# Kernel tuning notes

Hardware: AMD Instinct MI355X
Metric: run time of the kernel (lower is better)

## Reference

```python
import jax, jax.numpy as jnp
import numpy as np
from jax import lax

B, L, H = 2, 2048, 768
I = 2 * H            # intermediate_size = 1536
N = 16               # ssm state size
DT_RANK = 48         # ceil(H / 16)
K = 4                # conv kernel


def setup_inputs() -> dict:
    key = jax.random.key(0)
    ks = jax.random.split(key, 10)
    s = lambda fan_in: 1.0 / np.sqrt(fan_in)
    inp = {
        "input_states": jax.random.normal(ks[0], (B, L, H), jnp.float32),
        "in_proj_w": jax.random.normal(ks[1], (H, 2 * I), jnp.float32) * s(H),
        "conv_w": jax.random.normal(ks[2], (I, 1, K), jnp.float32) * s(K),
        "conv_b": jax.random.normal(ks[3], (I,), jnp.float32) * 0.02,
        "x_proj_w": jax.random.normal(ks[4], (I, DT_RANK + 2 * N), jnp.float32) * s(I),
        "dt_proj_w": jax.random.normal(ks[5], (DT_RANK, I), jnp.float32) * s(DT_RANK),
        "dt_proj_b": jax.random.normal(ks[6], (I,), jnp.float32) * 0.1,
        "A_log": jnp.log(jnp.broadcast_to(jnp.arange(1, N + 1, dtype=jnp.float32), (I, N))),
        "D_param": jnp.ones((I,), jnp.float32),
        "out_proj_w": jax.random.normal(ks[7], (I, H), jnp.float32) * s(I),
    }
    return inp


def reference(input_states, in_proj_w, conv_w, conv_b, x_proj_w,
              dt_proj_w, dt_proj_b, A_log, D_param, out_proj_w):
    dtype = input_states.dtype
    # in_proj -> [B, 2I, L], split into hidden and gate
    proj = jnp.einsum("blh,hj->bjl", input_states, in_proj_w)
    hidden, gate = jnp.split(proj, 2, axis=1)              # each [B, I, L]
    # causal depthwise conv1d (padding K-1 then truncate to L == left pad)
    k = conv_w.shape[-1]
    conv_out = lax.conv_general_dilated(
        hidden, conv_w, window_strides=(1,), padding=[(k - 1, 0)],
        feature_group_count=hidden.shape[1],
        dimension_numbers=("NCH", "OIH", "NCH"))
    hidden = jax.nn.silu(conv_out + conv_b[None, :, None])  # [B, I, L]
    # x_proj: [B, L, dt_rank + 2N]
    ssm_p = jnp.einsum("bil,ij->blj", hidden, x_proj_w)
    time_step = ssm_p[..., :DT_RANK]
    Bm = ssm_p[..., DT_RANK:DT_RANK + N]                    # [B, L, N]
    Cm = ssm_p[..., DT_RANK + N:]                           # [B, L, N]
    dt = jax.nn.softplus(time_step @ dt_proj_w + dt_proj_b)  # [B, L, I]
    dt = jnp.transpose(dt, (0, 2, 1))                        # [B, I, L]
    A = -jnp.exp(A_log.astype(jnp.float32))                  # [I, N]
    discrete_A = jnp.exp(A[None, :, None, :] * dt[:, :, :, None])        # [B,I,L,N]
    deltaB_u = (dt[:, :, :, None] * Bm[:, None, :, :].astype(jnp.float32)
                * hidden[:, :, :, None].astype(jnp.float32))             # [B,I,L,N]

    def step(state, x):
        dA_t, dBu_t = x
        new_state = dA_t * state + dBu_t
        return new_state, new_state

    init = jnp.zeros((hidden.shape[0], hidden.shape[1], N), jnp.float32)
    _, states = lax.scan(step, init,
                         (jnp.moveaxis(discrete_A, 2, 0),
                          jnp.moveaxis(deltaB_u, 2, 0)))    # [L, B, I, N]
    y = jnp.einsum("lbin,bln->bil", states, Cm.astype(jnp.float32)).astype(dtype)
    y = y + hidden * D_param[None, :, None]
    y = y * jax.nn.silu(gate)
    return jnp.einsum("bil,ih->blh", y, out_proj_w)
```

## Files before the change

kernel.cpp:

```cpp
#include <hip/hip_runtime.h>
#include <hip/hip_bf16.h>
#include <math.h>

#define B_ 2
#define L_ 2048
#define H_ 768
#define I_ 1536
#define J2 3072
#define KSPLIT 12
#define KCH (I_ / KSPLIT)
#define LC 16
#define NC (L_ / LC)

typedef __bf16 bf16x8 __attribute__((ext_vector_type(8)));
typedef float  f32x4  __attribute__((ext_vector_type(4)));

__device__ __forceinline__ float sigmoidf_(float x) { return 1.f / (1.f + __expf(-x)); }

__global__ __launch_bounds__(256) void pk_cvt(const float* __restrict__ src,
                                              __bf16* __restrict__ dst, int n8)
{
    int idx = blockIdx.x * 256 + threadIdx.x;
    if (idx >= n8) return;
    const float4* s = (const float4*)(src + (size_t)idx * 8);
    float4 a = s[0], b = s[1];
    bf16x8 v = {(__bf16)a.x,(__bf16)a.y,(__bf16)a.z,(__bf16)a.w,
                (__bf16)b.x,(__bf16)b.y,(__bf16)b.z,(__bf16)b.w};
    *(bf16x8*)(dst + (size_t)idx * 8) = v;
}

__global__ __launch_bounds__(256) void pk_tr(const float* __restrict__ src,
    __bf16* __restrict__ dst, int R, int C)
{
    __shared__ float tile[64][65];
    const int c0 = blockIdx.x * 64, r0 = blockIdx.y * 64;
    const int t = threadIdx.x;
    const int cc = t & 63, r4 = t >> 6;
#pragma unroll
    for (int q = 0; q < 16; ++q) {
        int r = r0 + q * 4 + r4;
        if (r < R && c0 + cc < C)
            tile[q * 4 + r4][cc] = src[(size_t)r * C + c0 + cc];
    }
    __syncthreads();
#pragma unroll
    for (int q = 0; q < 16; ++q) {
        int c = c0 + q * 4 + r4;
        if (c < C && r0 + cc < R)
            dst[(size_t)c * R + r0 + cc] = (__bf16)tile[cc][q * 4 + r4];
    }
}

__global__ __launch_bounds__(256) void pk_dtw(const float* __restrict__ dtW,
    __bf16* __restrict__ dtWT)
{
    int idx = blockIdx.x * 256 + threadIdx.x;
    if (idx >= I_ * 64) return;
    int i = idx >> 6, r = idx & 63;
    dtWT[idx] = (r < 48) ? (__bf16)dtW[(size_t)r * I_ + i] : (__bf16)0.f;
}

__global__ __launch_bounds__(256) void k1_mfma(const __bf16* __restrict__ Abf,
    const __bf16* __restrict__ WT, __bf16* __restrict__ preH16, __bf16* __restrict__ g16)
{
    __shared__ __align__(16) char smem[20480];
    __bf16* As = (__bf16*)smem;
    __bf16* Bs = As + 128 * 40;
    const int t = threadIdx.x;
    const int lane = t & 63, w = t >> 6;
    const int wr = w >> 1, wc = w & 1;
    const int m0 = blockIdx.y * 128, n0 = blockIdx.x * 128;
    const int l16 = lane & 15, kb = (lane >> 4) * 8;
    const int arow = t >> 1, ahalf = (t & 1) * 16;
    f32x4 acc[4][4] = {};

    for (int k0 = 0; k0 < H_; k0 += 32) {
        {
            const bf16x8* ap = (const bf16x8*)(Abf + (size_t)(m0 + arow) * H_ + k0 + ahalf);
            *(bf16x8*)&As[arow * 40 + ahalf] = ap[0];
            *(bf16x8*)&As[arow * 40 + ahalf + 8] = ap[1];
            const bf16x8* bp = (const bf16x8*)(WT + (size_t)(n0 + arow) * H_ + k0 + ahalf);
            *(bf16x8*)&Bs[arow * 40 + ahalf] = bp[0];
            *(bf16x8*)&Bs[arow * 40 + ahalf + 8] = bp[1];
        }
        __syncthreads();
        bf16x8 aF[4], bF[4];
#pragma unroll
        for (int mi = 0; mi < 4; ++mi)
            aF[mi] = *(const bf16x8*)&As[(wr * 64 + mi * 16 + l16) * 40 + kb];
#pragma unroll
        for (int ni = 0; ni < 4; ++ni)
            bF[ni] = *(const bf16x8*)&Bs[(wc * 64 + ni * 16 + l16) * 40 + kb];
#pragma unroll
        for (int mi = 0; mi < 4; ++mi)
#pragma unroll
            for (int ni = 0; ni < 4; ++ni)
                acc[mi][ni] = __builtin_amdgcn_mfma_f32_16x16x32_bf16(aF[mi], bF[ni], acc[mi][ni], 0, 0, 0);
        __syncthreads();
    }

    float* slab = (float*)smem + w * 1088;
    const int jtile = n0 + wc * 64;
    const int rm = lane >> 2, jb = (lane & 3) * 16;
    __bf16* outb = (jtile < I_) ? preH16 : g16;
    const int jg = (jtile < I_) ? jtile + jb : jtile - I_ + jb;
#pragma unroll
    for (int mi = 0; mi < 4; ++mi) {
#pragma unroll
        for (int ni = 0; ni < 4; ++ni)
#pragma unroll
            for (int r = 0; r < 4; ++r)
                slab[((lane >> 4) * 4 + r) * 68 + ni * 16 + l16] = acc[mi][ni][r];
        float v[16];
#pragma unroll
        for (int q = 0; q < 16; ++q) v[q] = slab[rm * 68 + jb + q];
        const size_t m = (size_t)m0 + wr * 64 + mi * 16 + rm;
        bf16x8 p0 = {(__bf16)v[0],(__bf16)v[1],(__bf16)v[2],(__bf16)v[3],
                     (__bf16)v[4],(__bf16)v[5],(__bf16)v[6],(__bf16)v[7]};
        bf16x8 p1 = {(__bf16)v[8],(__bf16)v[9],(__bf16)v[10],(__bf16)v[11],
                     (__bf16)v[12],(__bf16)v[13],(__bf16)v[14],(__bf16)v[15]};
        *(bf16x8*)(outb + m * I_ + jg) = p0;
        *(bf16x8*)(outb + m * I_ + jg + 8) = p1;
    }
}

__global__ __launch_bounds__(256) void k2conv(const __bf16* __restrict__ pre,
    const float* __restrict__ cw, const float* __restrict__ cb, __bf16* __restrict__ actT)
{
    __shared__ __bf16 in[67][72];
    const int i0 = blockIdx.x * 64, m0 = blockIdx.y * 64;
    const int l0 = m0 & (L_ - 1);
    const int t = threadIdx.x;
    const int ic = t & 63, r4 = t >> 6;
#pragma unroll
    for (int q = 0; q < 17; ++q) {
        int idx = t + 256 * q;
        if (idx < 67 * 64) {
            int row = idx >> 6, col = idx & 63;
            int lr = l0 - 3 + row;
            __bf16 v = (__bf16)0.f;
            if (lr >= 0)
                v = pre[(size_t)(m0 - 3 + row) * I_ + i0 + col];
            in[row][col] = v;
        }
    }
    __syncthreads();
    const int i = i0 + ic;
    float w0 = cw[i * 4 + 0], w1 = cw[i * 4 + 1], w2 = cw[i * 4 + 2], w3 = cw[i * 4 + 3];
    float bias = cb[i];
#pragma unroll
    for (int q = 0; q < 16; ++q) {
        int mr = q * 4 + r4;
        float s = bias + w0 * (float)in[mr][ic] + w1 * (float)in[mr + 1][ic]
                       + w2 * (float)in[mr + 2][ic] + w3 * (float)in[mr + 3][ic];
        actT[(size_t)(m0 + mr) * I_ + i] = (__bf16)(s * sigmoidf_(s));
    }
}

__global__ __launch_bounds__(256) void k3_split(const __bf16* __restrict__ At,
    const __bf16* __restrict__ XWT, float* __restrict__ part)
{
    __shared__ __align__(16) __bf16 As[64 * 40];
    __shared__ __align__(16) __bf16 Bs[80 * 40];
    const int t = threadIdx.x;
    const int lane = t & 63, w = t >> 6;
    const int m0 = blockIdx.x * 64;
    const int ks = blockIdx.y;
    const int l16 = lane & 15, kb = (lane >> 4) * 8;
    const int arow = t >> 2, aq = (t & 3) * 8;
    f32x4 acc[5] = {};

    for (int k0 = ks * KCH; k0 < (ks + 1) * KCH; k0 += 32) {
        *(bf16x8*)&As[arow * 40 + aq] =
            *(const bf16x8*)(At + (size_t)(m0 + arow) * I_ + k0 + aq);
        if (t < 160) {
            int j = t >> 1, ah = (t & 1) * 16;
            const bf16x8* bp = (const bf16x8*)(XWT + (size_t)j * I_ + k0 + ah);
            *(bf16x8*)&Bs[j * 40 + ah] = bp[0];
            *(bf16x8*)&Bs[j * 40 + ah + 8] = bp[1];
        }
        __syncthreads();
        bf16x8 aF = *(const bf16x8*)&As[(w * 16 + l16) * 40 + kb];
#pragma unroll
        for (int ni = 0; ni < 5; ++ni) {
            bf16x8 bF = *(const bf16x8*)&Bs[(ni * 16 + l16) * 40 + kb];
            acc[ni] = __builtin_amdgcn_mfma_f32_16x16x32_bf16(aF, bF, acc[ni], 0, 0, 0);
        }
        __syncthreads();
    }
    const int mrow = m0 + w * 16 + (lane >> 4) * 4;
    float* pp = part + (size_t)ks * ((size_t)B_ * L_ * 80);
#pragma unroll
    for (int ni = 0; ni < 5; ++ni)
#pragma unroll
        for (int r = 0; r < 4; ++r)
            pp[(size_t)(mrow + r) * 80 + ni * 16 + l16] = acc[ni][r];
}

__global__ __launch_bounds__(256) void k3_reduce(const float* __restrict__ part,
    __bf16* __restrict__ ssm16, float* __restrict__ Bpf, float* __restrict__ Cpf)
{
    int idx = blockIdx.x * 256 + threadIdx.x;
    if (idx >= B_ * L_ * 80) return;
    int m = idx / 80, j = idx - m * 80;
    float s = 0.f;
#pragma unroll
    for (int ks = 0; ks < KSPLIT; ++ks)
        s += part[(size_t)ks * ((size_t)B_ * L_ * 80) + idx];
    if (j < 48) {
        ssm16[(size_t)m * 64 + j] = (__bf16)s;
    } else {
        int n = j & 15;
        if (j < 64) {
            Bpf[(size_t)m * 16 + n] = s;
        } else {
            Cpf[(size_t)m * 16 + n] = s;
            ssm16[(size_t)m * 64 + (j - 16)] = (__bf16)0.f;
        }
    }
}

__global__ __launch_bounds__(256) void k4_mfma(const __bf16* __restrict__ S16,
    const __bf16* __restrict__ dtWT, const float* __restrict__ dtb, __bf16* __restrict__ dt)
{
    __shared__ __align__(16) __bf16 As[128 * 72];
    __shared__ __align__(16) __bf16 Bs[128 * 72];
    const int t = threadIdx.x;
    const int lane = t & 63, w = t >> 6;
    const int wr = w >> 1, wc = w & 1;
    const int m0 = blockIdx.y * 128, n0 = blockIdx.x * 128;
    const int l16 = lane & 15, kq8 = (lane >> 4) * 8;
    {
        const int row = t >> 1, off = (t & 1) * 32;
        const bf16x8* ap = (const bf16x8*)(S16 + (size_t)(m0 + row) * 64 + off);
        *(bf16x8*)&As[row * 72 + off]      = ap[0];
        *(bf16x8*)&As[row * 72 + off + 8]  = ap[1];
        *(bf16x8*)&As[row * 72 + off + 16] = ap[2];
        *(bf16x8*)&As[row * 72 + off + 24] = ap[3];
        const bf16x8* bp = (const bf16x8*)(dtWT + (size_t)(n0 + row) * 64 + off);
        *(bf16x8*)&Bs[row * 72 + off]      = bp[0];
        *(bf16x8*)&Bs[row * 72 + off + 8]  = bp[1];
        *(bf16x8*)&Bs[row * 72 + off + 16] = bp[2];
        *(bf16x8*)&Bs[row * 72 + off + 24] = bp[3];
    }
    __syncthreads();
    f32x4 acc[4][4] = {};
#pragma unroll
    for (int ks = 0; ks < 2; ++ks) {
        const int kb = ks * 32 + kq8;
        bf16x8 aF[4], bF[4];
#pragma unroll
        for (int mi = 0; mi < 4; ++mi)
            aF[mi] = *(const bf16x8*)&As[(wr * 64 + mi * 16 + l16) * 72 + kb];
#pragma unroll
        for (int ni = 0; ni < 4; ++ni)
            bF[ni] = *(const bf16x8*)&Bs[(wc * 64 + ni * 16 + l16) * 72 + kb];
#pragma unroll
        for (int mi = 0; mi < 4; ++mi)
#pragma unroll
            for (int ni = 0; ni < 4; ++ni)
                acc[mi][ni] = __builtin_amdgcn_mfma_f32_16x16x32_bf16(aF[mi], bF[ni], acc[mi][ni], 0, 0, 0);
    }
    const int mbase = m0 + wr * 64 + (lane >> 4) * 4;
    const int nbase = n0 + wc * 64 + l16;
#pragma unroll
    for (int ni = 0; ni < 4; ++ni) {
        const int i = nbase + ni * 16;
        const float bias = dtb[i];
#pragma unroll
        for (int mi = 0; mi < 4; ++mi)
#pragma unroll
            for (int r = 0; r < 4; ++r) {
                float x = acc[mi][ni][r] + bias;
                float sp = (x > 20.f) ? x : log1pf(__expf(x));
                dt[(size_t)(mbase + mi * 16 + r) * I_ + i] = (__bf16)sp;
            }
    }
}

__global__ __launch_bounds__(256) void k5a(const __bf16* __restrict__ dt,
    const __bf16* __restrict__ hT, const float* __restrict__ Bpf,
    float* __restrict__ Ebuf, float* __restrict__ Pbuf)
{
    const int mc = blockIdx.x;
    const int b = mc >> 7, c = mc & (NC - 1);
    const int it = blockIdx.y * 256 + threadIdx.x;
    const int ch = b * I_ + it;
    const size_t mrow0 = (size_t)b * L_ + (size_t)c * LC;

    float s[16];
#pragma unroll
    for (int n = 0; n < 16; ++n) s[n] = 0.f;
    float sumd = 0.f;

    for (int ll = 0; ll < LC; ++ll) {
        const size_t m = mrow0 + ll;
        float d = (float)dt[m * I_ + it];
        float h = (float)hT[m * I_ + it];
        f32x4 B0 = *(const f32x4*)(Bpf + m * 16);
        f32x4 B1 = *(const f32x4*)(Bpf + m * 16 + 4);
        f32x4 B2 = *(const f32x4*)(Bpf + m * 16 + 8);
        f32x4 B3 = *(const f32x4*)(Bpf + m * 16 + 12);
        float u = d * h;
        float e1 = __expf(-d);
        float e2 = e1 * e1, e4 = e2 * e2, e8 = e4 * e4;
        float dA[16];
        dA[0] = e1; dA[1] = e2; dA[2] = e2 * e1; dA[3] = e4;
#pragma unroll
        for (int n = 0; n < 4; ++n) dA[4 + n] = dA[n] * e4;
#pragma unroll
        for (int n = 0; n < 8; ++n) dA[8 + n] = dA[n] * e8;
        sumd += d;
#pragma unroll
        for (int n = 0; n < 16; ++n) {
            float Bn = (n < 4) ? B0[n] : (n < 8) ? B1[n - 4] : (n < 12) ? B2[n - 8] : B3[n - 12];
            s[n] = fmaf(dA[n], s[n], u * Bn);
        }
    }
#pragma unroll
    for (int n = 0; n < 16; ++n)
        Ebuf[(size_t)(c * 16 + n) * J2 + ch] = s[n];
    Pbuf[(size_t)c * J2 + ch] = __expf(-sumd);
}

__global__ __launch_bounds__(256) void k5b(float* __restrict__ Ebuf,
    const float* __restrict__ Pbuf)
{
    const int n = blockIdx.x / (J2 / 256);
    const int ch = (blockIdx.x % (J2 / 256)) * 256 + threadIdx.x;
    const int e = n + 1;
    float run = 0.f;
    for (int c = 0; c < NC; ++c) {
        float E = Ebuf[(size_t)(c * 16 + n) * J2 + ch];
        float f1 = Pbuf[(size_t)c * J2 + ch];
        float pw = 1.f, base = f1;
        int ee = e;
#pragma unroll
        for (int k = 0; k < 5; ++k) {
            if (ee & 1) pw *= base;
            base *= base;
            ee >>= 1;
        }
        Ebuf[(size_t)(c * 16 + n) * J2 + ch] = run;
        run = fmaf(pw, run, E);
    }
}

__global__ __launch_bounds__(256) void k5c(const __bf16* __restrict__ dt,
    __bf16* hyT, const __bf16* __restrict__ g16,
    const float* __restrict__ Bpf, const float* __restrict__ Cpf,
    const float* __restrict__ Ebuf, const float* __restrict__ Dp)
{
    const int mc = blockIdx.x;
    const int b = mc >> 7, c = mc & (NC - 1);
    const int it = blockIdx.y * 256 + threadIdx.x;
    const int ch = b * I_ + it;
    const size_t mrow0 = (size_t)b * L_ + (size_t)c * LC;
    const float D = Dp[it];

    float s[16];
#pragma unroll
    for (int n = 0; n < 16; ++n)
        s[n] = Ebuf[(size_t)(c * 16 + n) * J2 + ch];

    for (int ll = 0; ll < LC; ++ll) {
        const size_t m = mrow0 + ll;
        float d = (float)dt[m * I_ + it];
        float h = (float)hyT[m * I_ + it];
        f32x4 B0 = *(const f32x4*)(Bpf + m * 16);
        f32x4 B1 = *(const f32x4*)(Bpf + m * 16 + 4);
        f32x4 B2 = *(const f32x4*)(Bpf + m * 16 + 8);
        f32x4 B3 = *(const f32x4*)(Bpf + m * 16 + 12);
        f32x4 C0 = *(const f32x4*)(Cpf + m * 16);
        f32x4 C1 = *(const f32x4*)(Cpf + m * 16 + 4);
        f32x4 C2 = *(const f32x4*)(Cpf + m * 16 + 8);
        f32x4 C3 = *(const f32x4*)(Cpf + m * 16 + 12);
        float u = d * h;
        float e1 = __expf(-d);
        float e2 = e1 * e1, e4 = e2 * e2, e8 = e4 * e4;
        float dA[16];
        dA[0] = e1; dA[1] = e2; dA[2] = e2 * e1; dA[3] = e4;
#pragma unroll
        for (int n = 0; n < 4; ++n) dA[4 + n] = dA[n] * e4;
#pragma unroll
        for (int n = 0; n < 8; ++n) dA[8 + n] = dA[n] * e8;
        float a0 = D * h, a1 = 0.f, a2 = 0.f, a3 = 0.f;
#pragma unroll
        for (int n = 0; n < 4; ++n) {
            s[n]      = fmaf(dA[n],      s[n],      u * B0[n]);
            s[n + 4]  = fmaf(dA[n + 4],  s[n + 4],  u * B1[n]);
            s[n + 8]  = fmaf(dA[n + 8],  s[n + 8],  u * B2[n]);
            s[n + 12] = fmaf(dA[n + 12], s[n + 12], u * B3[n]);
            a0 = fmaf(s[n],      C0[n], a0);
            a1 = fmaf(s[n + 4],  C1[n], a1);
            a2 = fmaf(s[n + 8],  C2[n], a2);
            a3 = fmaf(s[n + 12], C3[n], a3);
        }
        float y = (a0 + a1) + (a2 + a3);
        float g = (float)g16[m * I_ + it];
        hyT[m * I_ + it] = (__bf16)(y * g * sigmoidf_(g));
    }
}

__global__ __launch_bounds__(256) void k6_mfma(const __bf16* __restrict__ Yt,
    const __bf16* __restrict__ WoT, float* __restrict__ out)
{
    __shared__ __align__(16) __bf16 As[64 * 40];
    __shared__ __align__(16) __bf16 Bs[64 * 40];
    const int t = threadIdx.x;
    const int lane = t & 63, w = t >> 6;
    const int wr = w >> 1, wc = w & 1;
    const int m0 = blockIdx.y * 64, n0 = blockIdx.x * 64;
    const int l16 = lane & 15, kb = (lane >> 4) * 8;
    const int arow = t >> 2, aq = (t & 3) * 8;
    f32x4 acc[2][2] = {};

    for (int k0 = 0; k0 < I_; k0 += 32) {
        *(bf16x8*)&As[arow * 40 + aq] =
            *(const bf16x8*)(Yt + (size_t)(m0 + arow) * I_ + k0 + aq);
        *(bf16x8*)&Bs[arow * 40 + aq] =
            *(const bf16x8*)(WoT + (size_t)(n0 + arow) * I_ + k0 + aq);
        __syncthreads();
        bf16x8 aF[2], bF[2];
#pragma unroll
        for (int mi = 0; mi < 2; ++mi)
            aF[mi] = *(const bf16x8*)&As[(wr * 32 + mi * 16 + l16) * 40 + kb];
#pragma unroll
        for (int ni = 0; ni < 2; ++ni)
            bF[ni] = *(const bf16x8*)&Bs[(wc * 32 + ni * 16 + l16) * 40 + kb];
#pragma unroll
        for (int mi = 0; mi < 2; ++mi)
#pragma unroll
            for (int ni = 0; ni < 2; ++ni)
                acc[mi][ni] = __builtin_amdgcn_mfma_f32_16x16x32_bf16(aF[mi], bF[ni], acc[mi][ni], 0, 0, 0);
        __syncthreads();
    }
    const int mbase = m0 + wr * 32 + (lane >> 4) * 4;
    const int nbase = n0 + wc * 32 + l16;
#pragma unroll
    for (int mi = 0; mi < 2; ++mi)
#pragma unroll
        for (int ni = 0; ni < 2; ++ni)
#pragma unroll
            for (int r = 0; r < 4; ++r)
                out[(size_t)(mbase + mi * 16 + r) * H_ + nbase + ni * 16] = acc[mi][ni][r];
}

extern "C" void kernel_launch(void* const* d_in, const int* in_sizes, int n_in,
                              void* d_out, int out_size, void* d_ws, size_t ws_size,
                              hipStream_t stream)
{
    const float* in_states  = (const float*)d_in[0];
    const float* in_proj_w  = (const float*)d_in[1];
    const float* conv_w     = (const float*)d_in[2];
    const float* conv_b     = (const float*)d_in[3];
    const float* x_proj_w   = (const float*)d_in[4];
    const float* dt_proj_w  = (const float*)d_in[5];
    const float* dt_proj_b  = (const float*)d_in[6];
    const float* D_param    = (const float*)d_in[8];
    const float* out_proj_w = (const float*)d_in[9];
    float* out = (float*)d_out;

    const size_t CH = (size_t)B_ * I_ * L_;
    const size_t ML = (size_t)B_ * L_;

    char* ws = (char*)d_ws;
    __bf16* dt16  = (__bf16*)ws;
    __bf16* Abf   = (__bf16*)ws;
    __bf16* W1T   = Abf + (size_t)ML * H_;
    char* p = ws + CH * 4;
    __bf16* preH16 = (__bf16*)p;  p += CH * 2;
    __bf16* g16    = (__bf16*)p;  p += CH * 2;
    __bf16* actT   = (__bf16*)p;  p += CH * 2;
    __bf16* ssm16  = (__bf16*)p;  p += ML * 64 * 2;
    float*  Ebuf   = (float*)p;
    float*  part   = (float*)p;
    float*  Pbuf   = Ebuf + (size_t)NC * 16 * J2; p += ((size_t)NC * 16 * J2 + (size_t)NC * J2) * 4;
    __bf16* WoT    = (__bf16*)p;  p += (size_t)H_ * I_ * 2;
    __bf16* XWT    = (__bf16*)p;  p += (size_t)80 * I_ * 2;
    __bf16* dtWT   = (__bf16*)p;  p += (size_t)I_ * 64 * 2;
    float*  Bpf    = (float*)p;   p += ML * 16 * 4;
    float*  Cpf    = (float*)p;

    hipLaunchKernelGGL(pk_cvt, dim3((int)((ML * H_ / 8 + 255) / 256)), dim3(256), 0, stream,
                       in_states, Abf, (int)(ML * H_ / 8));
    hipLaunchKernelGGL(pk_tr, dim3(J2 / 64, H_ / 64), dim3(256), 0, stream,
                       in_proj_w, W1T, H_, J2);
    hipLaunchKernelGGL(pk_tr, dim3(H_ / 64, I_ / 64), dim3(256), 0, stream,
                       out_proj_w, WoT, I_, H_);
    hipLaunchKernelGGL(pk_tr, dim3(2, I_ / 64), dim3(256), 0, stream,
                       x_proj_w, XWT, I_, 80);
    hipLaunchKernelGGL(pk_dtw, dim3((I_ * 64 + 255) / 256), dim3(256), 0, stream,
                       dt_proj_w, dtWT);

    hipLaunchKernelGGL(k1_mfma, dim3(J2 / 128, ML / 128), dim3(256), 0, stream,
                       Abf, W1T, preH16, g16);
    hipLaunchKernelGGL(k2conv, dim3(I_ / 64, ML / 64), dim3(256), 0, stream,
                       preH16, conv_w, conv_b, actT);
    hipLaunchKernelGGL(k3_split, dim3(ML / 64, KSPLIT), dim3(256), 0, stream,
                       actT, XWT, part);
    hipLaunchKernelGGL(k3_reduce, dim3((int)((ML * 80 + 255) / 256)), dim3(256), 0, stream,
                       part, ssm16, Bpf, Cpf);
    hipLaunchKernelGGL(k4_mfma, dim3(I_ / 128, ML / 128), dim3(256), 0, stream,
                       ssm16, dtWT, dt_proj_b, dt16);
    hipLaunchKernelGGL(k5a, dim3(B_ * NC, I_ / 256), dim3(256), 0, stream,
                       dt16, actT, Bpf, Ebuf, Pbuf);
    hipLaunchKernelGGL(k5b, dim3(16 * (J2 / 256)), dim3(256), 0, stream,
                       Ebuf, Pbuf);
    hipLaunchKernelGGL(k5c, dim3(B_ * NC, I_ / 256), dim3(256), 0, stream,
                       dt16, actT, g16, Bpf, Cpf, Ebuf, D_param);
    hipLaunchKernelGGL(k6_mfma, dim3(H_ / 64, ML / 64), dim3(256), 0, stream,
                       actT, WoT, out);
}
```

Measured before the change: 218.9 us.

## Merge weight prep kernels, swizzle GEMM tiles, and double scan chunk length

```diff
diff --git a/kernel.cpp b/kernel.cpp
--- a/kernel.cpp
+++ b/kernel.cpp
@@ -9,7 +9,7 @@
 #define J2 3072
 #define KSPLIT 12
 #define KCH (I_ / KSPLIT)
-#define LC 16
+#define LC 32
 #define NC (L_ / LC)
 
 typedef __bf16 bf16x8 __attribute__((ext_vector_type(8)));
@@ -17,24 +17,10 @@
 
 __device__ __forceinline__ float sigmoidf_(float x) { return 1.f / (1.f + __expf(-x)); }
 
-__global__ __launch_bounds__(256) void pk_cvt(const float* __restrict__ src,
-                                              __bf16* __restrict__ dst, int n8)
-{
-    int idx = blockIdx.x * 256 + threadIdx.x;
-    if (idx >= n8) return;
-    const float4* s = (const float4*)(src + (size_t)idx * 8);
-    float4 a = s[0], b = s[1];
-    bf16x8 v = {(__bf16)a.x,(__bf16)a.y,(__bf16)a.z,(__bf16)a.w,
-                (__bf16)b.x,(__bf16)b.y,(__bf16)b.z,(__bf16)b.w};
-    *(bf16x8*)(dst + (size_t)idx * 8) = v;
-}
-
-__global__ __launch_bounds__(256) void pk_tr(const float* __restrict__ src,
-    __bf16* __restrict__ dst, int R, int C)
-{
-    __shared__ float tile[64][65];
-    const int c0 = blockIdx.x * 64, r0 = blockIdx.y * 64;
-    const int t = threadIdx.x;
+__device__ __forceinline__ void tr_tile_(const float* __restrict__ src,
+    __bf16* __restrict__ dst, int R, int C, int bx, int by, int t, float (*tile)[65])
+{
+    const int c0 = bx * 64, r0 = by * 64;
     const int cc = t & 63, r4 = t >> 6;
 #pragma unroll
     for (int q = 0; q < 16; ++q) {
@@ -51,13 +37,36 @@
     }
 }
 
-__global__ __launch_bounds__(256) void pk_dtw(const float* __restrict__ dtW,
-    __bf16* __restrict__ dtWT)
-{
-    int idx = blockIdx.x * 256 + threadIdx.x;
-    if (idx >= I_ * 64) return;
-    int i = idx >> 6, r = idx & 63;
-    dtWT[idx] = (r < 48) ? (__bf16)dtW[(size_t)r * I_ + i] : (__bf16)0.f;
+__global__ __launch_bounds__(256) void pk_all(
+    const float* __restrict__ in_states, __bf16* __restrict__ Abf,
+    const float* __restrict__ in_proj_w, __bf16* __restrict__ W1T,
+    const float* __restrict__ out_proj_w, __bf16* __restrict__ WoT,
+    const float* __restrict__ x_proj_w, __bf16* __restrict__ XWT,
+    const float* __restrict__ dt_proj_w, __bf16* __restrict__ dtWT)
+{
+    __shared__ float tile[64][65];
+    const int bb = blockIdx.x, t = threadIdx.x;
+    if (bb < 1536) {
+        int idx = bb * 256 + t;
+        const float4* s = (const float4*)(in_states + (size_t)idx * 8);
+        float4 a = s[0], b = s[1];
+        bf16x8 v = {(__bf16)a.x,(__bf16)a.y,(__bf16)a.z,(__bf16)a.w,
+                    (__bf16)b.x,(__bf16)b.y,(__bf16)b.z,(__bf16)b.w};
+        *(bf16x8*)(Abf + (size_t)idx * 8) = v;
+    } else if (bb < 2112) {
+        int idx = bb - 1536;
+        tr_tile_(in_proj_w, W1T, H_, J2, idx % 48, idx / 48, t, tile);
+    } else if (bb < 2400) {
+        int idx = bb - 2112;
+        tr_tile_(out_proj_w, WoT, I_, H_, idx % 12, idx / 12, t, tile);
+    } else if (bb < 2448) {
+        int idx = bb - 2400;
+        tr_tile_(x_proj_w, XWT, I_, 80, idx % 2, idx / 2, t, tile);
+    } else {
+        int idx = (bb - 2448) * 256 + t;
+        int i = idx >> 6, r = idx & 63;
+        dtWT[idx] = (r < 48) ? (__bf16)dt_proj_w[(size_t)r * I_ + i] : (__bf16)0.f;
+    }
 }
 
 __global__ __launch_bounds__(256) void k1_mfma(const __bf16* __restrict__ Abf,
@@ -69,7 +78,9 @@
     const int t = threadIdx.x;
     const int lane = t & 63, w = t >> 6;
     const int wr = w >> 1, wc = w & 1;
-    const int m0 = blockIdx.y * 128, n0 = blockIdx.x * 128;
+    const int flat = blockIdx.y * 24 + blockIdx.x;
+    const int swz = (flat & 7) * 96 + (flat >> 3);
+    const int m0 = (swz / 24) * 128, n0 = (swz % 24) * 128;
     const int l16 = lane & 15, kb = (lane >> 4) * 8;
     const int arow = t >> 1, ahalf = (t & 1) * 16;
     f32x4 acc[4][4] = {};
@@ -283,7 +294,7 @@
     float* __restrict__ Ebuf, float* __restrict__ Pbuf)
 {
     const int mc = blockIdx.x;
-    const int b = mc >> 7, c = mc & (NC - 1);
+    const int b = mc / NC, c = mc & (NC - 1);
     const int it = blockIdx.y * 256 + threadIdx.x;
     const int ch = b * I_ + it;
     const size_t mrow0 = (size_t)b * L_ + (size_t)c * LC;
@@ -352,7 +363,7 @@
     const float* __restrict__ Ebuf, const float* __restrict__ Dp)
 {
     const int mc = blockIdx.x;
-    const int b = mc >> 7, c = mc & (NC - 1);
+    const int b = mc / NC, c = mc & (NC - 1);
     const int it = blockIdx.y * 256 + threadIdx.x;
     const int ch = b * I_ + it;
     const size_t mrow0 = (size_t)b * L_ + (size_t)c * LC;
@@ -410,7 +421,9 @@
     const int t = threadIdx.x;
     const int lane = t & 63, w = t >> 6;
     const int wr = w >> 1, wc = w & 1;
-    const int m0 = blockIdx.y * 64, n0 = blockIdx.x * 64;
+    const int flat = blockIdx.y * 12 + blockIdx.x;
+    const int swz = (flat & 7) * 96 + (flat >> 3);
+    const int m0 = (swz / 12) * 64, n0 = (swz % 12) * 64;
     const int l16 = lane & 15, kb = (lane >> 4) * 8;
     const int arow = t >> 2, aq = (t & 3) * 8;
     f32x4 acc[2][2] = {};
@@ -475,23 +488,17 @@
     __bf16* ssm16  = (__bf16*)p;  p += ML * 64 * 2;
     float*  Ebuf   = (float*)p;
     float*  part   = (float*)p;
-    float*  Pbuf   = Ebuf + (size_t)NC * 16 * J2; p += ((size_t)NC * 16 * J2 + (size_t)NC * J2) * 4;
+    float*  Pbuf   = Ebuf + (size_t)NC * 16 * J2;
+    p += (size_t)KSPLIT * ML * 80 * 4;
     __bf16* WoT    = (__bf16*)p;  p += (size_t)H_ * I_ * 2;
     __bf16* XWT    = (__bf16*)p;  p += (size_t)80 * I_ * 2;
     __bf16* dtWT   = (__bf16*)p;  p += (size_t)I_ * 64 * 2;
     float*  Bpf    = (float*)p;   p += ML * 16 * 4;
     float*  Cpf    = (float*)p;
 
-    hipLaunchKernelGGL(pk_cvt, dim3((int)((ML * H_ / 8 + 255) / 256)), dim3(256), 0, stream,
-                       in_states, Abf, (int)(ML * H_ / 8));
-    hipLaunchKernelGGL(pk_tr, dim3(J2 / 64, H_ / 64), dim3(256), 0, stream,
-                       in_proj_w, W1T, H_, J2);
-    hipLaunchKernelGGL(pk_tr, dim3(H_ / 64, I_ / 64), dim3(256), 0, stream,
-                       out_proj_w, WoT, I_, H_);
-    hipLaunchKernelGGL(pk_tr, dim3(2, I_ / 64), dim3(256), 0, stream,
-                       x_proj_w, XWT, I_, 80);
-    hipLaunchKernelGGL(pk_dtw, dim3((I_ * 64 + 255) / 256), dim3(256), 0, stream,
-                       dt_proj_w, dtWT);
+    hipLaunchKernelGGL(pk_all, dim3(2832), dim3(256), 0, stream,
+                       in_states, Abf, in_proj_w, W1T, out_proj_w, WoT,
+                       x_proj_w, XWT, dt_proj_w, dtWT);
 
     hipLaunchKernelGGL(k1_mfma, dim3(J2 / 128, ML / 128), dim3(256), 0, stream,
                        Abf, W1T, preH16, g16);
```

Result: faster. 179.3 us (-18.1%).
